# Optimization experiments

Measured on AMD Instinct MI355X. Metric: run time of the kernel, lower is better.

The kernel has to match this reference:

```python
import jax, jax.numpy as jnp
import numpy as np

TEMPERATURE = 1.0        # sample_codebook_temperature
COMMITMENT_COST = 1.0

B, T, D, K = 8, 4096, 64, 1024


def setup_inputs() -> dict:
    key = jax.random.key(0)
    k1, k2 = jax.random.split(key)
    x = jax.random.normal(k1, (B, T, D), dtype=jnp.float32)
    embeddings = jax.random.normal(k2, (D, K), dtype=jnp.float32)  # (embedding_dim, codebook_size)
    return {"x": x, "embeddings": embeddings}


def gumbel_softmax(logits, temperature):
    # logits: [N, K]
    K_ = logits.shape[1]
    indices = jnp.argmax(logits, axis=1)
    enc = jax.nn.one_hot(indices, K_, dtype=logits.dtype)
    pi0 = jax.nn.softmax(logits, axis=-1)
    pi1 = (enc + jax.nn.softmax(logits / temperature, axis=-1)) / 2
    pi1 = jax.nn.softmax(jax.lax.stop_gradient(jnp.log(pi1) - logits), axis=1)
    pi2 = 2 * pi1 - 0.5 * pi0
    encodings = pi2 - jax.lax.stop_gradient(pi2) + enc  # straight-through encodings
    return indices, encodings


def reference(x, embeddings):
    D_, K_ = embeddings.shape
    flat = x.reshape(-1, D_)                              # [N, D]
    # squared euclidean distances via matmul (cdist trick)
    sim = flat @ embeddings                               # [N, K]
    dist = (jnp.sum(flat ** 2, axis=1, keepdims=True)
            - 2.0 * sim
            + jnp.sum(embeddings ** 2, axis=0, keepdims=True))
    indices, encodings = gumbel_softmax(-dist, TEMPERATURE)
    indices = indices.reshape(x.shape[:-1])               # [B, T]
    quantized = embeddings.T[indices]                     # gather: [B, T, D]
    e_latent_loss = jnp.mean(jnp.square(jax.lax.stop_gradient(quantized) - x))
    loss = e_latent_loss * COMMITMENT_COST
    # straight-through estimator (training-mode output; same values as eval)
    quantized = x + jax.lax.stop_gradient(quantized - x)
    return quantized, encodings, indices, loss
```

## Files before the change

kernel.cpp:

```cpp
#include <hip/hip_runtime.h>
#include <hip/hip_bf16.h>


#define NROWS 32768
#define DDIM  64
#define KCB   1024
#define NSEG  8
#define SEG   128

typedef float f32x4 __attribute__((ext_vector_type(4)));

#define WS_ET    0
#define WS_H     65536
#define WS_PART  66560
#define WS_IBEST 66688
#define WS_PBEST 99456
#define WS_PIDX  361600

__global__ __launch_bounds__(256) void k1_prep(const float* __restrict__ E,
                                               float* __restrict__ Et,
                                               float* __restrict__ h) {
  int k = blockIdx.x * 256 + threadIdx.x;
  float col[DDIM];
  float sum = 0.f;
#pragma unroll
  for (int d = 0; d < DDIM; ++d) {
    float v = E[d * KCB + k];
    col[d] = v;
    sum = fmaf(v, v, sum);
  }
  float4* dst = (float4*)(Et + (size_t)k * DDIM);
#pragma unroll
  for (int i = 0; i < 16; ++i)
    dst[i] = make_float4(col[4*i], col[4*i+1], col[4*i+2], col[4*i+3]);
  h[k] = 0.5f * sum;
}

__global__ __launch_bounds__(256, 3) void k2_score(const float* __restrict__ x,
                                                   const float* __restrict__ Et,
                                                   const float* __restrict__ h,
                                                   float* __restrict__ pbest,
                                                   unsigned short* __restrict__ pidx) {
  __shared__ float se[SEG * DDIM];
  __shared__ float sh[SEG];

  int bid = blockIdx.x;
  int ks  = bid >> 7;
  int tid = threadIdx.x;
  int n   = (bid & 127) * 256 + tid;

  {
    const float4* src = (const float4*)(Et + (size_t)ks * SEG * DDIM);
    float4* dst = (float4*)se;
#pragma unroll
    for (int i = 0; i < 8; ++i) {
      int f = tid + i * 256;
      dst[f] = src[f];
    }
    if (tid < SEG) sh[tid] = h[ks * SEG + tid];
  }

  const float4* xr = (const float4*)(x + (size_t)n * DDIM);
  float4 xv[16];
#pragma unroll
  for (int i = 0; i < 16; ++i) xv[i] = xr[i];
  asm volatile("" ::: "memory");
  __syncthreads();

  float best = -3.0e38f;
  int besti = ks * SEG;

#pragma unroll 1
  for (int kg = 0; kg < SEG; kg += 8) {
    float acc[8];
#pragma unroll
    for (int j = 0; j < 8; ++j) acc[j] = -sh[kg + j];
#pragma unroll
    for (int i = 0; i < 16; ++i) {
      float4 xi = xv[i];
#pragma unroll
      for (int j = 0; j < 8; ++j) {
        float4 e4 = *(const float4*)(se + (kg + j) * DDIM + i * 4);
        acc[j] = fmaf(xi.x, e4.x, acc[j]);
        acc[j] = fmaf(xi.y, e4.y, acc[j]);
        acc[j] = fmaf(xi.z, e4.z, acc[j]);
        acc[j] = fmaf(xi.w, e4.w, acc[j]);
      }
    }
#pragma unroll
    for (int j = 0; j < 8; ++j) {
      if (acc[j] > best) { best = acc[j]; besti = ks * SEG + kg + j; }
    }
  }
  pbest[ks * NROWS + n] = best;
  pidx [ks * NROWS + n] = (unsigned short)besti;
}

__global__ __launch_bounds__(256) void k3_rows(const float* __restrict__ x,
                                               const float* __restrict__ Et,
                                               const float* __restrict__ pbest,
                                               const unsigned short* __restrict__ pidx,
                                               int* __restrict__ ibest,
                                               float* __restrict__ partial,
                                               float* __restrict__ out_q,
                                               float* __restrict__ out_ind) {
  int n = blockIdx.x * 256 + threadIdx.x;
  float best = pbest[n];
  int bi = pidx[n];
#pragma unroll
  for (int q = 1; q < NSEG; ++q) {
    float b = pbest[q * NROWS + n];
    int i2 = (int)pidx[q * NROWS + n];
    if (b > best) { best = b; bi = i2; }
  }
  ibest[n] = bi;
  out_ind[n] = (float)bi;

  const float4* xr = (const float4*)(x + (size_t)n * DDIM);
  const float4* qr = (const float4*)(Et + (size_t)bi * DDIM);
  float4* qw = (float4*)(out_q + (size_t)n * DDIM);
  float lsum = 0.f;
#pragma unroll
  for (int i = 0; i < 16; ++i) {
    float4 q4 = qr[i];
    float4 x4 = xr[i];
    float d0 = q4.x - x4.x, d1 = q4.y - x4.y, d2 = q4.z - x4.z, d3 = q4.w - x4.w;
    lsum = fmaf(d0, d0, lsum); lsum = fmaf(d1, d1, lsum);
    lsum = fmaf(d2, d2, lsum); lsum = fmaf(d3, d3, lsum);
    qw[i] = q4;
  }

#pragma unroll
  for (int off = 32; off > 0; off >>= 1) lsum += __shfl_down(lsum, off);
  __shared__ float red[4];
  int lane = threadIdx.x & 63, w = threadIdx.x >> 6;
  if (lane == 0) red[w] = lsum;
  __syncthreads();
  if (threadIdx.x == 0) partial[blockIdx.x] = red[0] + red[1] + red[2] + red[3];
}

__global__ __launch_bounds__(256) void k4_enc(const int* __restrict__ ibest,
                                              float* __restrict__ out_enc) {
  int t = threadIdx.x;
  int r0 = blockIdx.x * 16;
  int idx[16];
#pragma unroll
  for (int r = 0; r < 16; ++r) idx[r] = ibest[r0 + r];
#pragma unroll
  for (int r = 0; r < 16; ++r) {
    f32x4 v = (f32x4)(0.f);
    if ((idx[r] >> 2) == t) v[idx[r] & 3] = 1.0f;
    __builtin_nontemporal_store(v, (f32x4*)(out_enc + (size_t)(r0 + r) * KCB + t * 4));
  }
}

__global__ void k5_loss(const float* __restrict__ partial, float* __restrict__ out_loss) {
  int t = threadIdx.x;
  float s = partial[t] + partial[t + 64];
#pragma unroll
  for (int off = 32; off > 0; off >>= 1) s += __shfl_down(s, off);
  if (t == 0) out_loss[0] = s * (1.0f / 2097152.0f);
}

extern "C" void kernel_launch(void* const* d_in, const int* in_sizes, int n_in,
                              void* d_out, int out_size, void* d_ws, size_t ws_size,
                              hipStream_t stream) {
  const float* x = (const float*)d_in[0];
  const float* E = (const float*)d_in[1];

  float* ws    = (float*)d_ws;
  float* Et    = ws + WS_ET;
  float* h     = ws + WS_H;
  float* part  = ws + WS_PART;
  int*   ibest = (int*)(ws + WS_IBEST);
  float* pbest = ws + WS_PBEST;
  unsigned short* pidx = (unsigned short*)(ws + WS_PIDX);

  float* out      = (float*)d_out;
  float* out_q    = out;
  float* out_enc  = out + 2097152;
  float* out_ind  = out + 35651584;
  float* out_loss = out + 35684352;

  k1_prep<<<4, 256, 0, stream>>>(E, Et, h);
  k2_score<<<1024, 256, 0, stream>>>(x, Et, h, pbest, pidx);
  k3_rows<<<128, 256, 0, stream>>>(x, Et, pbest, pidx, ibest, part, out_q, out_ind);
  k4_enc<<<2048, 256, 0, stream>>>(ibest, out_enc);
  k5_loss<<<1, 64, 0, stream>>>(part, out_loss);
}
```

Baseline: 246.4 us.

## Register-block two rows per thread in scoring and fuse gather with one-hot writes

The scoring kernel now has each thread compute distances for two rows against the same shared-memory codebook entries, halving LDS reads per FMA, with launch bounds relaxed to two waves per SIMD. The per-row argmin merge, quantized gather, loss partials and one-hot encoding store are fused into one kernel over 16-row blocks, removing the ibest workspace round trip and one launch. The loss reduction kernel is widened to sum 2048 partials. Costs include higher register pressure and fewer blocks in the scoring kernel, plus a serial 16-thread merge step at the start of each fused block.

```diff
diff --git a/kernel.cpp b/kernel.cpp
--- a/kernel.cpp
+++ b/kernel.cpp
@@ -13,9 +13,8 @@
 #define WS_ET    0
 #define WS_H     65536
 #define WS_PART  66560
-#define WS_IBEST 66688
-#define WS_PBEST 99456
-#define WS_PIDX  361600
+#define WS_PBEST 68608
+#define WS_PIDX  330752
 
 __global__ __launch_bounds__(256) void k1_prep(const float* __restrict__ E,
                                                float* __restrict__ Et,
@@ -36,7 +35,7 @@
   h[k] = 0.5f * sum;
 }
 
-__global__ __launch_bounds__(256, 3) void k2_score(const float* __restrict__ x,
+__global__ __launch_bounds__(256, 2) void k2_score(const float* __restrict__ x,
                                                    const float* __restrict__ Et,
                                                    const float* __restrict__ h,
                                                    float* __restrict__ pbest,
@@ -45,121 +44,133 @@
   __shared__ float sh[SEG];
 
   int bid = blockIdx.x;
-  int ks  = bid >> 7;
+  int ks  = bid >> 6;
   int tid = threadIdx.x;
-  int n   = (bid & 127) * 256 + tid;
+  int n0  = (bid & 63) * 512 + tid;
 
   {
     const float4* src = (const float4*)(Et + (size_t)ks * SEG * DDIM);
     float4* dst = (float4*)se;
 #pragma unroll
-    for (int i = 0; i < 8; ++i) {
-      int f = tid + i * 256;
-      dst[f] = src[f];
-    }
+    for (int i = 0; i < 8; ++i) dst[tid + i * 256] = src[tid + i * 256];
     if (tid < SEG) sh[tid] = h[ks * SEG + tid];
   }
 
-  const float4* xr = (const float4*)(x + (size_t)n * DDIM);
-  float4 xv[16];
+  const float4* xra = (const float4*)(x + (size_t)n0 * DDIM);
+  const float4* xrb = (const float4*)(x + (size_t)(n0 + 256) * DDIM);
+  float4 xa[16], xb[16];
 #pragma unroll
-  for (int i = 0; i < 16; ++i) xv[i] = xr[i];
-  asm volatile("" ::: "memory");
+  for (int i = 0; i < 16; ++i) { xa[i] = xra[i]; xb[i] = xrb[i]; }
+#pragma unroll
+  for (int i = 0; i < 16; ++i) {
+    asm volatile("" :: "v"(xa[i].x), "v"(xa[i].y), "v"(xa[i].z), "v"(xa[i].w));
+    asm volatile("" :: "v"(xb[i].x), "v"(xb[i].y), "v"(xb[i].z), "v"(xb[i].w));
+  }
   __syncthreads();
 
-  float best = -3.0e38f;
-  int besti = ks * SEG;
+  float bestA = -3.0e38f, bestB = -3.0e38f;
+  int ia = ks * SEG, ib = ks * SEG;
 
 #pragma unroll 1
-  for (int kg = 0; kg < SEG; kg += 8) {
-    float acc[8];
+  for (int kg = 0; kg < SEG; kg += 4) {
+    float accA[4], accB[4];
 #pragma unroll
-    for (int j = 0; j < 8; ++j) acc[j] = -sh[kg + j];
+    for (int j = 0; j < 4; ++j) { float hn = -sh[kg + j]; accA[j] = hn; accB[j] = hn; }
 #pragma unroll
     for (int i = 0; i < 16; ++i) {
-      float4 xi = xv[i];
+      float4 xia = xa[i], xib = xb[i];
 #pragma unroll
-      for (int j = 0; j < 8; ++j) {
+      for (int j = 0; j < 4; ++j) {
         float4 e4 = *(const float4*)(se + (kg + j) * DDIM + i * 4);
-        acc[j] = fmaf(xi.x, e4.x, acc[j]);
-        acc[j] = fmaf(xi.y, e4.y, acc[j]);
-        acc[j] = fmaf(xi.z, e4.z, acc[j]);
-        acc[j] = fmaf(xi.w, e4.w, acc[j]);
+        accA[j] = fmaf(xia.x, e4.x, accA[j]);
+        accA[j] = fmaf(xia.y, e4.y, accA[j]);
+        accA[j] = fmaf(xia.z, e4.z, accA[j]);
+        accA[j] = fmaf(xia.w, e4.w, accA[j]);
+        accB[j] = fmaf(xib.x, e4.x, accB[j]);
+        accB[j] = fmaf(xib.y, e4.y, accB[j]);
+        accB[j] = fmaf(xib.z, e4.z, accB[j]);
+        accB[j] = fmaf(xib.w, e4.w, accB[j]);
       }
     }
 #pragma unroll
-    for (int j = 0; j < 8; ++j) {
-      if (acc[j] > best) { best = acc[j]; besti = ks * SEG + kg + j; }
+    for (int j = 0; j < 4; ++j) {
+      if (accA[j] > bestA) { bestA = accA[j]; ia = ks * SEG + kg + j; }
+      if (accB[j] > bestB) { bestB = accB[j]; ib = ks * SEG + kg + j; }
     }
   }
-  pbest[ks * NROWS + n] = best;
-  pidx [ks * NROWS + n] = (unsigned short)besti;
+  pbest[ks * NROWS + n0]       = bestA;
+  pidx [ks * NROWS + n0]       = (unsigned short)ia;
+  pbest[ks * NROWS + n0 + 256] = bestB;
+  pidx [ks * NROWS + n0 + 256] = (unsigned short)ib;
 }
 
-__global__ __launch_bounds__(256) void k3_rows(const float* __restrict__ x,
-                                               const float* __restrict__ Et,
-                                               const float* __restrict__ pbest,
-                                               const unsigned short* __restrict__ pidx,
-                                               int* __restrict__ ibest,
-                                               float* __restrict__ partial,
-                                               float* __restrict__ out_q,
-                                               float* __restrict__ out_ind) {
-  int n = blockIdx.x * 256 + threadIdx.x;
-  float best = pbest[n];
-  int bi = pidx[n];
+__global__ __launch_bounds__(256) void k34_fused(const float* __restrict__ x,
+                                                 const float* __restrict__ Et,
+                                                 const float* __restrict__ pbest,
+                                                 const unsigned short* __restrict__ pidx,
+                                                 float* __restrict__ partial,
+                                                 float* __restrict__ out_q,
+                                                 float* __restrict__ out_enc,
+                                                 float* __restrict__ out_ind) {
+  __shared__ int sidx[16];
+  int tid = threadIdx.x;
+  int r0 = blockIdx.x * 16;
+
+  if (tid < 16) {
+    int n = r0 + tid;
+    float best = pbest[n];
+    int bi = pidx[n];
 #pragma unroll
-  for (int q = 1; q < NSEG; ++q) {
-    float b = pbest[q * NROWS + n];
-    int i2 = (int)pidx[q * NROWS + n];
-    if (b > best) { best = b; bi = i2; }
+    for (int q = 1; q < NSEG; ++q) {
+      float b = pbest[q * NROWS + n];
+      int i2 = (int)pidx[q * NROWS + n];
+      if (b > best) { best = b; bi = i2; }
+    }
+    sidx[tid] = bi;
+    out_ind[n] = (float)bi;
   }
-  ibest[n] = bi;
-  out_ind[n] = (float)bi;
+  __syncthreads();
 
-  const float4* xr = (const float4*)(x + (size_t)n * DDIM);
-  const float4* qr = (const float4*)(Et + (size_t)bi * DDIM);
-  float4* qw = (float4*)(out_q + (size_t)n * DDIM);
+  int r = tid >> 4, c = tid & 15;
+  int n = r0 + r;
+  int bi = sidx[r];
+  float4 q4 = *(const float4*)(Et + (size_t)bi * DDIM + c * 4);
+  float4 x4 = *(const float4*)(x + (size_t)n * DDIM + c * 4);
+  float d0 = q4.x - x4.x, d1 = q4.y - x4.y, d2 = q4.z - x4.z, d3 = q4.w - x4.w;
   float lsum = 0.f;
+  lsum = fmaf(d0, d0, lsum); lsum = fmaf(d1, d1, lsum);
+  lsum = fmaf(d2, d2, lsum); lsum = fmaf(d3, d3, lsum);
+  *(float4*)(out_q + (size_t)n * DDIM + c * 4) = q4;
+
 #pragma unroll
-  for (int i = 0; i < 16; ++i) {
-    float4 q4 = qr[i];
-    float4 x4 = xr[i];
-    float d0 = q4.x - x4.x, d1 = q4.y - x4.y, d2 = q4.z - x4.z, d3 = q4.w - x4.w;
-    lsum = fmaf(d0, d0, lsum); lsum = fmaf(d1, d1, lsum);
-    lsum = fmaf(d2, d2, lsum); lsum = fmaf(d3, d3, lsum);
-    qw[i] = q4;
+  for (int rr = 0; rr < 16; ++rr) {
+    int bk = sidx[rr];
+    f32x4 v = (f32x4)(0.f);
+    if ((bk >> 2) == tid) v[bk & 3] = 1.0f;
+    __builtin_nontemporal_store(v, (f32x4*)(out_enc + (size_t)(r0 + rr) * KCB + tid * 4));
   }
 
 #pragma unroll
   for (int off = 32; off > 0; off >>= 1) lsum += __shfl_down(lsum, off);
   __shared__ float red[4];
-  int lane = threadIdx.x & 63, w = threadIdx.x >> 6;
+  int lane = tid & 63, w = tid >> 6;
   if (lane == 0) red[w] = lsum;
   __syncthreads();
-  if (threadIdx.x == 0) partial[blockIdx.x] = red[0] + red[1] + red[2] + red[3];
-}
-
-__global__ __launch_bounds__(256) void k4_enc(const int* __restrict__ ibest,
-                                              float* __restrict__ out_enc) {
-  int t = threadIdx.x;
-  int r0 = blockIdx.x * 16;
-  int idx[16];
-#pragma unroll
-  for (int r = 0; r < 16; ++r) idx[r] = ibest[r0 + r];
-#pragma unroll
-  for (int r = 0; r < 16; ++r) {
-    f32x4 v = (f32x4)(0.f);
-    if ((idx[r] >> 2) == t) v[idx[r] & 3] = 1.0f;
-    __builtin_nontemporal_store(v, (f32x4*)(out_enc + (size_t)(r0 + r) * KCB + t * 4));
-  }
+  if (tid == 0) partial[blockIdx.x] = red[0] + red[1] + red[2] + red[3];
 }
 
 __global__ void k5_loss(const float* __restrict__ partial, float* __restrict__ out_loss) {
   int t = threadIdx.x;
-  float s = partial[t] + partial[t + 64];
+  float s = 0.f;
+#pragma unroll
+  for (int i = 0; i < 8; ++i) s += partial[t + i * 256];
 #pragma unroll
   for (int off = 32; off > 0; off >>= 1) s += __shfl_down(s, off);
-  if (t == 0) out_loss[0] = s * (1.0f / 2097152.0f);
+  __shared__ float red[4];
+  int lane = t & 63, w = t >> 6;
+  if (lane == 0) red[w] = s;
+  __syncthreads();
+  if (t == 0) out_loss[0] = (red[0] + red[1] + red[2] + red[3]) * (1.0f / 2097152.0f);
 }
 
 extern "C" void kernel_launch(void* const* d_in, const int* in_sizes, int n_in,
@@ -172,7 +183,6 @@
   float* Et    = ws + WS_ET;
   float* h     = ws + WS_H;
   float* part  = ws + WS_PART;
-  int*   ibest = (int*)(ws + WS_IBEST);
   float* pbest = ws + WS_PBEST;
   unsigned short* pidx = (unsigned short*)(ws + WS_PIDX);
 
@@ -183,8 +193,7 @@
   float* out_loss = out + 35684352;
 
   k1_prep<<<4, 256, 0, stream>>>(E, Et, h);
-  k2_score<<<1024, 256, 0, stream>>>(x, Et, h, pbest, pidx);
-  k3_rows<<<128, 256, 0, stream>>>(x, Et, pbest, pidx, ibest, part, out_q, out_ind);
-  k4_enc<<<2048, 256, 0, stream>>>(ibest, out_enc);
-  k5_loss<<<1, 64, 0, stream>>>(part, out_loss);
+  k2_score<<<512, 256, 0, stream>>>(x, Et, h, pbest, pidx);
+  k34_fused<<<2048, 256, 0, stream>>>(x, Et, pbest, pidx, part, out_q, out_enc, out_ind);
+  k5_loss<<<1, 256, 0, stream>>>(part, out_loss);
 }
```

After: 264.6 us. 1.07x slower.
